# Kernel optimization log

Hardware: AMD Instinct MI355X
Metric: run time of the kernel (lower is better)

The kernel has to match this reference:

```python
import jax, jax.numpy as jnp
import numpy as np

B, N, DIM = 4, 4096, 1024
HEADS, DIM_HEAD, BSZ, EPS = 8, 64, 16, 1e-8
INNER = HEADS * DIM_HEAD


def setup_inputs() -> dict:
    key = jax.random.key(0)
    k1, k2, k3 = jax.random.split(key, 3)
    x = jax.random.normal(k1, (B, N, DIM), dtype=jnp.float32)
    # torch nn.Linear weights are [out, in]; scale ~ fan_in^-0.5 for stable exp()
    w_qkv = jax.random.normal(k2, (3 * INNER, DIM), dtype=jnp.float32) * (DIM ** -0.5)
    w_out = jax.random.normal(k3, (DIM, INNER), dtype=jnp.float32) * (INNER ** -0.5)
    b_out = jnp.zeros((DIM,), dtype=jnp.float32)
    return {"x": x, "w_qkv": w_qkv, "w_out": w_out, "b_out": b_out}


def _to_bh(t, b, n):
    # 'b n (h d) -> (b h) n d'
    return t.reshape(b, n, HEADS, DIM_HEAD).transpose(0, 2, 1, 3).reshape(b * HEADS, n, DIM_HEAD)


def _to_blocks(t):
    # 'b (n z) d -> b n z d'
    return t.reshape(t.shape[0], -1, BSZ, DIM_HEAD)


def _calc_Y_and_A(qb, kb, vb):
    S = jnp.einsum('bnid,bnjd->bnij', qb, kb)   # block-local scores
    A = jnp.exp(S)
    y = jnp.einsum('bnij,bnjd->bnid', A, vb)
    return y.reshape(y.shape[0], -1, DIM_HEAD), A.sum(-1).reshape(A.shape[0], -1)


def _hattention(x, w_qkv, w_out, b_out):
    b, n, _ = x.shape
    qkv = x @ w_qkv.T
    q, k, v = jnp.split(qkv, 3, axis=-1)
    q, k, v = (_to_bh(t, b, n) for t in (q, k, v))
    q = q * (DIM_HEAD ** -0.5)

    num_levels = int(np.log2(n // BSZ)) - 1
    qkvs = [(q, k, v)]
    for _ in range(num_levels):
        q = q.reshape(q.shape[0], -1, 2, DIM_HEAD).mean(axis=2)
        k = k.reshape(k.shape[0], -1, 2, DIM_HEAD).mean(axis=2)
        v = v.reshape(v.shape[0], -1, 2, DIM_HEAD).sum(axis=2)
        qkvs.append((q, k, v))
    top_level = qkvs[0]
    coarse_levels = qkvs[1:][::-1]  # coarsest first

    Ys = []
    for (ql, kl, vl) in coarse_levels:
        qb, kb, vb = map(_to_blocks, (ql, kl, vl))
        bh, nb = kb.shape[0], kb.shape[1]
        # flip sibling key blocks: 'b (n r) z d' with r=2 reversed
        kb = kb.reshape(bh, nb // 2, 2, BSZ, DIM_HEAD)[:, :, ::-1].reshape(bh, nb, BSZ, DIM_HEAD)
        Ys.append(_calc_Y_and_A(qb, kb, vb))
    Ys.append(_calc_Y_and_A(*map(_to_blocks, top_level)))

    Y, A = Ys[0]
    for y_l, a_l in Ys[1:]:
        Y = jnp.repeat(Y, 2, axis=1) + y_l
        A = jnp.repeat(A, 2, axis=1) + a_l

    out = Y / (A + EPS)[..., None]
    # '(b h) n d -> b n (h d)'
    out = out.reshape(b, HEADS, n, DIM_HEAD).transpose(0, 2, 1, 3).reshape(b, n, INNER)
    return out @ w_out.T + b_out


def reference(x, w_qkv, w_out, b_out):
    return _hattention(x, w_qkv, w_out, b_out)
```

## Files before the change

### kernel.cpp

```cpp
#include <hip/hip_runtime.h>
#include <hip/hip_bf16.h>


typedef __bf16 bf16x8 __attribute__((ext_vector_type(8)));
typedef float floatx4 __attribute__((ext_vector_type(4)));
typedef unsigned short ushortx8 __attribute__((ext_vector_type(8)));
typedef unsigned int uintx4 __attribute__((ext_vector_type(4)));

#define ROWS_PER_BH 8160

__device__ __forceinline__ void g2lds16(const void* g, void* l) {
  __builtin_amdgcn_global_load_lds(
      (const __attribute__((address_space(1))) void*)g,
      (__attribute__((address_space(3))) void*)l, 16, 0, 0);
}

__device__ __forceinline__ unsigned short f2bu(float x) {
  __hip_bfloat16 h = __float2bfloat16(x);
  return *(unsigned short*)&h;
}
__device__ __forceinline__ float bu2f(unsigned short u) {
  __hip_bfloat16 h = *(__hip_bfloat16*)&u;
  return __bfloat162float(h);
}

__global__ __launch_bounds__(256) void f2b3_kernel(const float* __restrict__ x,
                                                   const float* __restrict__ wq,
                                                   const float* __restrict__ wo,
                                                   __hip_bfloat16* __restrict__ xb,
                                                   __hip_bfloat16* __restrict__ wqb,
                                                   __hip_bfloat16* __restrict__ wob) {
  int i0 = (blockIdx.x * 256 + threadIdx.x) * 4;
  const float* s;
  __hip_bfloat16* d;
  if (i0 < 16777216) {
    s = x; d = xb;
  } else if (i0 < 16777216 + 1572864) {
    s = wq + (i0 - 16777216); d = wqb + (i0 - 16777216); i0 = 0;
    float4 v = *(const float4*)s;
    d[0] = __float2bfloat16(v.x); d[1] = __float2bfloat16(v.y);
    d[2] = __float2bfloat16(v.z); d[3] = __float2bfloat16(v.w);
    return;
  } else {
    s = wo + (i0 - 16777216 - 1572864); d = wob + (i0 - 16777216 - 1572864);
    float4 v = *(const float4*)s;
    d[0] = __float2bfloat16(v.x); d[1] = __float2bfloat16(v.y);
    d[2] = __float2bfloat16(v.z); d[3] = __float2bfloat16(v.w);
    return;
  }
  float4 v = *(const float4*)(s + i0);
  d[i0 + 0] = __float2bfloat16(v.x);
  d[i0 + 1] = __float2bfloat16(v.y);
  d[i0 + 2] = __float2bfloat16(v.z);
  d[i0 + 3] = __float2bfloat16(v.w);
}

template <int K>
__device__ __forceinline__ void gemm_core(const unsigned short* __restrict__ A,
                                          const unsigned short* __restrict__ B,
                                          unsigned short* ldsA, unsigned short* ldsB,
                                          int tM, int tN, floatx4 acc[4][4]) {
  const int tid = threadIdx.x;
  const int lane = tid & 63, w = tid >> 6;
  const int wm = w >> 1, wn = w & 1;
  const int lr = lane >> 3;
  const int gch = (lane & 7) ^ lr;
  const unsigned short* Ag = A + (size_t)(tM + w * 32 + lr) * K + gch * 8;
  const unsigned short* Bg = B + (size_t)(tN + w * 32 + lr) * K + gch * 8;
  unsigned short* lA = &ldsA[w * 2048 + lane * 8];
  unsigned short* lB = &ldsB[w * 2048 + lane * 8];

  const int rA = wm * 64 + (lane & 15);
  const int rB = wn * 64 + (lane & 15);
  const int quad = lane >> 4;
  const int sw = lane & 7;

  for (int kt = 0; kt < K; kt += 64) {
    __syncthreads();
#pragma unroll
    for (int c = 0; c < 4; c++) {
      g2lds16(Ag + (size_t)(c * 8) * K + kt, lA + c * 512);
      g2lds16(Bg + (size_t)(c * 8) * K + kt, lB + c * 512);
    }
    __syncthreads();
#pragma unroll
    for (int kk = 0; kk < 2; kk++) {
      bf16x8 af[4], bv[4];
#pragma unroll
      for (int i = 0; i < 4; i++)
        af[i] = *(const bf16x8*)&ldsA[(rA + i * 16) * 64 + (((kk * 4 + quad) ^ sw) * 8)];
#pragma unroll
      for (int j = 0; j < 4; j++)
        bv[j] = *(const bf16x8*)&ldsB[(rB + j * 16) * 64 + (((kk * 4 + quad) ^ sw) * 8)];
#pragma unroll
      for (int i = 0; i < 4; i++)
#pragma unroll
        for (int j = 0; j < 4; j++)
          acc[i][j] = __builtin_amdgcn_mfma_f32_16x16x32_bf16(af[i], bv[j], acc[i][j], 0, 0, 0);
    }
  }
}

__global__ __launch_bounds__(256) void gemm_qkv_kernel(
    const unsigned short* __restrict__ A,
    const unsigned short* __restrict__ B,
    __hip_bfloat16* __restrict__ qp, __hip_bfloat16* __restrict__ kp,
    __hip_bfloat16* __restrict__ vp) {
  __shared__ unsigned short ldsA[128 * 64];
  __shared__ unsigned short ldsB[128 * 64];
  const int lane = threadIdx.x & 63, w = threadIdx.x >> 6;
  const int wm = w >> 1, wn = w & 1;
  const int tM = blockIdx.x * 128, tN = blockIdx.y * 128;

  floatx4 acc[4][4];
#pragma unroll
  for (int i = 0; i < 4; i++)
#pragma unroll
    for (int j = 0; j < 4; j++) acc[i][j] = (floatx4){0.f, 0.f, 0.f, 0.f};

  gemm_core<1024>(A, B, ldsA, ldsB, tM, tN, acc);

  const int quad = lane >> 4;
#pragma unroll
  for (int i = 0; i < 4; i++) {
#pragma unroll
    for (int j = 0; j < 4; j++) {
      const int c = tN + wn * 64 + j * 16 + (lane & 15);
      const int tensor = c >> 9;
      const int rem = c & 511;
      const int h = rem >> 6, d = rem & 63;
      __hip_bfloat16* dstbuf = (tensor == 0) ? qp : ((tensor == 1) ? kp : vp);
      const float scale = (tensor == 0) ? 0.125f : 1.0f;
#pragma unroll
      for (int r = 0; r < 4; r++) {
        const int m = tM + wm * 64 + i * 16 + quad * 4 + r;
        const int b = m >> 12, n = m & 4095;
        size_t dst = ((size_t)(b * 8 + h) * ROWS_PER_BH + n) * 64 + d;
        dstbuf[dst] = __float2bfloat16(acc[i][j][r] * scale);
      }
    }
  }
}

__global__ __launch_bounds__(256) void gemm_out_kernel(
    const unsigned short* __restrict__ A,
    const unsigned short* __restrict__ B,
    const float* __restrict__ bias, float* __restrict__ out) {
  __shared__ unsigned short ldsA[128 * 64];
  __shared__ unsigned short ldsB[128 * 64];
  const int lane = threadIdx.x & 63, w = threadIdx.x >> 6;
  const int wm = w >> 1, wn = w & 1;
  const int tM = blockIdx.x * 128, tN = blockIdx.y * 128;

  floatx4 acc[4][4];
#pragma unroll
  for (int i = 0; i < 4; i++)
#pragma unroll
    for (int j = 0; j < 4; j++) acc[i][j] = (floatx4){0.f, 0.f, 0.f, 0.f};

  gemm_core<512>(A, B, ldsA, ldsB, tM, tN, acc);

  const int quad = lane >> 4;
#pragma unroll
  for (int i = 0; i < 4; i++) {
#pragma unroll
    for (int j = 0; j < 4; j++) {
      const int c = tN + wn * 64 + j * 16 + (lane & 15);
      const float bb = bias[c];
#pragma unroll
      for (int r = 0; r < 4; r++) {
        const int m = tM + wm * 64 + i * 16 + quad * 4 + r;
        out[(size_t)m * 1024 + c] = acc[i][j][r] + bb;
      }
    }
  }
}

__global__ __launch_bounds__(256) void pyramid_all_kernel(
    __hip_bfloat16* __restrict__ qp, __hip_bfloat16* __restrict__ kp,
    __hip_bfloat16* __restrict__ vp) {
  __shared__ unsigned short qs[128 * 64], ks[128 * 64], vs[128 * 64];
  const int bh = blockIdx.x >> 5;
  const int chunk = blockIdx.x & 31;
  const int tid = threadIdx.x;
  const size_t base = (size_t)bh * ROWS_PER_BH;
  const size_t g0 = (base + chunk * 128) * 64;
  const unsigned short* qg = (const unsigned short*)qp;
  const unsigned short* kg = (const unsigned short*)kp;
  const unsigned short* vg = (const unsigned short*)vp;
#pragma unroll
  for (int c = 0; c < 4; c++) {
    int off = c * 2048 + tid * 8;
    *(ushortx8*)&qs[off] = *(const ushortx8*)(qg + g0 + off);
    *(ushortx8*)&ks[off] = *(const ushortx8*)(kg + g0 + off);
    *(ushortx8*)&vs[off] = *(const ushortx8*)(vg + g0 + off);
  }
  const int offs[8] = {0, 4096, 6144, 7168, 7680, 7936, 8064, 8128};
#pragma unroll
  for (int l = 1; l <= 7; l++) {
    __syncthreads();
    const int nOut = 128 >> l;
    for (int e = tid; e < nOut * 32; e += 256) {
      const int i = e >> 5, dp = (e & 31) * 2;
      const int a = (i << l) * 64 + dp;
      const int b = a + (1 << (l - 1)) * 64;
      unsigned short q0 = f2bu(0.5f * (bu2f(qs[a]) + bu2f(qs[b])));
      unsigned short q1 = f2bu(0.5f * (bu2f(qs[a + 1]) + bu2f(qs[b + 1])));
      unsigned short k0 = f2bu(0.5f * (bu2f(ks[a]) + bu2f(ks[b])));
      unsigned short k1 = f2bu(0.5f * (bu2f(ks[a + 1]) + bu2f(ks[b + 1])));
      unsigned short v0 = f2bu(bu2f(vs[a]) + bu2f(vs[b]));
      unsigned short v1 = f2bu(bu2f(vs[a + 1]) + bu2f(vs[b + 1]));
      qs[a] = q0; qs[a + 1] = q1;
      ks[a] = k0; ks[a + 1] = k1;
      vs[a] = v0; vs[a + 1] = v1;
      const size_t grow = (base + offs[l] + (size_t)chunk * nOut + i) * 64 + dp;
      *(unsigned int*)((unsigned short*)qp + grow) = (unsigned int)q0 | ((unsigned int)q1 << 16);
      *(unsigned int*)((unsigned short*)kp + grow) = (unsigned int)k0 | ((unsigned int)k1 << 16);
      *(unsigned int*)((unsigned short*)vp + grow) = (unsigned int)v0 | ((unsigned int)v1 << 16);
    }
  }
}

__global__ __launch_bounds__(256) void attn_kernel(
    const unsigned short* __restrict__ qp, const unsigned short* __restrict__ kp,
    const unsigned short* __restrict__ vp, __hip_bfloat16* __restrict__ yall,
    float* __restrict__ aall) {
  __shared__ __align__(16) unsigned short vT[4][64 * 24];
  const int w = threadIdx.x >> 6, lane = threadIdx.x & 63;
  const int g = blockIdx.x * 4 + w;
  if (g >= 510) return;
  const int bh = blockIdx.y;
  int level, blk;
  if (g < 256)      { level = 0; blk = g; }
  else if (g < 384) { level = 1; blk = g - 256; }
  else if (g < 448) { level = 2; blk = g - 384; }
  else if (g < 480) { level = 3; blk = g - 448; }
  else if (g < 496) { level = 4; blk = g - 480; }
  else if (g < 504) { level = 5; blk = g - 496; }
  else if (g < 508) { level = 6; blk = g - 504; }
  else              { level = 7; blk = g - 508; }
  const int ro = 8192 - (8192 >> level);
  const int kblk = (level == 0) ? blk : (blk ^ 1);
  const int m = lane & 15, q = lane >> 4;
  const size_t qbase = ((size_t)bh * ROWS_PER_BH + ro + blk * 16) * 64;
  const size_t kbase = ((size_t)bh * ROWS_PER_BH + ro + kblk * 16) * 64;

  const bf16x8 ka0 = *(const bf16x8*)(kp + kbase + m * 64 + q * 8);
  const bf16x8 ka1 = *(const bf16x8*)(kp + kbase + m * 64 + 32 + q * 8);
  const bf16x8 qb0 = *(const bf16x8*)(qp + qbase + m * 64 + q * 8);
  const bf16x8 qb1 = *(const bf16x8*)(qp + qbase + m * 64 + 32 + q * 8);

  const ushortx8 v0 = *(const ushortx8*)(vp + qbase + m * 64 + q * 16);
  const ushortx8 v1 = *(const ushortx8*)(vp + qbase + m * 64 + q * 16 + 8);
  unsigned short* vtw = vT[w];
#pragma unroll
  for (int j = 0; j < 8; j++) vtw[(q * 16 + j) * 24 + m] = v0[j];
#pragma unroll
  for (int j = 0; j < 8; j++) vtw[(q * 16 + 8 + j) * 24 + m] = v1[j];

  floatx4 s = (floatx4){0.f, 0.f, 0.f, 0.f};
  s = __builtin_amdgcn_mfma_f32_16x16x32_bf16(ka0, qb0, s, 0, 0, 0);
  s = __builtin_amdgcn_mfma_f32_16x16x32_bf16(ka1, qb1, s, 0, 0, 0);

  unsigned short pb0 = f2bu(__expf(s[0])), pb1 = f2bu(__expf(s[1]));
  unsigned short pb2 = f2bu(__expf(s[2])), pb3 = f2bu(__expf(s[3]));
  float asum = bu2f(pb0) + bu2f(pb1) + bu2f(pb2) + bu2f(pb3);
  asum += __shfl_xor(asum, 16, 64);
  asum += __shfl_xor(asum, 32, 64);
  const size_t arow = (size_t)bh * ROWS_PER_BH + ro + blk * 16;
  if (q == 0) aall[arow + m] = asum;

  unsigned int d0 = (unsigned int)pb0 | ((unsigned int)pb1 << 16);
  unsigned int d1 = (unsigned int)pb2 | ((unsigned int)pb3 << 16);
  const int s0l = m + 32 * (q & 1);
  unsigned int u0 = __shfl(d0, s0l, 64);
  unsigned int u1 = __shfl(d1, s0l, 64);
  unsigned int u2 = __shfl(d0, s0l + 16, 64);
  unsigned int u3 = __shfl(d1, s0l + 16, 64);
  union { uintx4 i; bf16x8 b; } pau;
  pau.i = (q < 2) ? (uintx4){u0, u1, u2, u3} : (uintx4){0u, 0u, 0u, 0u};
  const bf16x8 pa = pau.b;

#pragma unroll
  for (int c = 0; c < 4; c++) {
    union { uintx4 i; bf16x8 b; } bvu;
    bvu.i = (uintx4){0u, 0u, 0u, 0u};
    if (q < 2) bvu.b = *(const bf16x8*)&vtw[(c * 16 + m) * 24 + q * 8];
    floatx4 y = (floatx4){0.f, 0.f, 0.f, 0.f};
    y = __builtin_amdgcn_mfma_f32_16x16x32_bf16(pa, bvu.b, y, 0, 0, 0);
#pragma unroll
    for (int r = 0; r < 4; r++)
      yall[(arow + q * 4 + r) * 64 + c * 16 + m] = __float2bfloat16(y[r]);
  }
}

__global__ __launch_bounds__(256) void combine_kernel(
    const unsigned short* __restrict__ yall, const float* __restrict__ aall,
    __hip_bfloat16* __restrict__ Ub) {
  int idx = blockIdx.x * 256 + threadIdx.x;
  int d4 = (idx & 15) * 4;
  int i = (idx >> 4) & 4095;
  int bh = idx >> 16;
  size_t base = (size_t)bh * ROWS_PER_BH;
  float Y0 = 0.f, Y1 = 0.f, Y2 = 0.f, Y3 = 0.f, Aa = 0.f;
#pragma unroll
  for (int l = 0; l < 8; l++) {
    int r = (8192 - (8192 >> l)) + (i >> l);
    uint2 yv = *(const uint2*)(yall + (base + r) * 64 + d4);
    Y0 += bu2f((unsigned short)(yv.x & 0xffff));
    Y1 += bu2f((unsigned short)(yv.x >> 16));
    Y2 += bu2f((unsigned short)(yv.y & 0xffff));
    Y3 += bu2f((unsigned short)(yv.y >> 16));
    Aa += aall[base + r];
  }
  float inv = 1.0f / (Aa + 1e-8f);
  unsigned int o0 = (unsigned int)f2bu(Y0 * inv) | ((unsigned int)f2bu(Y1 * inv) << 16);
  unsigned int o1 = (unsigned int)f2bu(Y2 * inv) | ((unsigned int)f2bu(Y3 * inv) << 16);
  int b = bh >> 3, h = bh & 7;
  size_t m = (size_t)b * 4096 + i;
  uint2 o = {o0, o1};
  *(uint2*)((unsigned short*)Ub + m * 512 + (size_t)h * 64 + d4) = o;
}

extern "C" void kernel_launch(void* const* d_in, const int* in_sizes, int n_in,
                              void* d_out, int out_size, void* d_ws, size_t ws_size,
                              hipStream_t stream) {
  const float* x     = (const float*)d_in[0];
  const float* w_qkv = (const float*)d_in[1];
  const float* w_out = (const float*)d_in[2];
  const float* b_out = (const float*)d_in[3];
  float* out = (float*)d_out;

  char* ws = (char*)d_ws;
  __hip_bfloat16* xb    = (__hip_bfloat16*)(ws + 0);
  __hip_bfloat16* wqkvb = (__hip_bfloat16*)(ws + 33554432);
  __hip_bfloat16* wob   = (__hip_bfloat16*)(ws + 36700160);
  __hip_bfloat16* qp    = (__hip_bfloat16*)(ws + 37748736);
  __hip_bfloat16* kp    = (__hip_bfloat16*)(ws + 71172096);
  __hip_bfloat16* vp    = (__hip_bfloat16*)(ws + 104595456);
  __hip_bfloat16* yall  = (__hip_bfloat16*)(ws + 138018816);
  float* aall           = (float*)(ws + 171442176);
  __hip_bfloat16* Ub    = (__hip_bfloat16*)(ws + 172486656);

  f2b3_kernel<<<18432, 256, 0, stream>>>(x, w_qkv, w_out, xb, wqkvb, wob);

  gemm_qkv_kernel<<<dim3(128, 12), 256, 0, stream>>>(
      (const unsigned short*)xb, (const unsigned short*)wqkvb, qp, kp, vp);

  pyramid_all_kernel<<<1024, 256, 0, stream>>>(qp, kp, vp);

  attn_kernel<<<dim3(128, 32), 256, 0, stream>>>(
      (const unsigned short*)qp, (const unsigned short*)kp,
      (const unsigned short*)vp, yall, aall);

  combine_kernel<<<8192, 256, 0, stream>>>((const unsigned short*)yall, aall, Ub);

  gemm_out_kernel<<<dim3(128, 8), 256, 0, stream>>>(
      (const unsigned short*)Ub, (const unsigned short*)wob, b_out, out);
}
```

Before: 264.7 us.

## Fuse fine pyramid levels, attention and combine into one LDS-resident kernel

The QKV GEMM epilogue now also writes level-4 (16-row mean/sum) pyramid rows directly using cross-lane shuffles. A small kernel builds levels 5-7 from those, a reduced attention kernel handles only coarse levels 4-7, and a new fused kernel loads a 256-row chunk per head into swizzled LDS, builds levels 1-3 in place, runs block attention for levels 0-3 and combines with the coarse results to write the normalized output. This removes the global round trips for fine pyramid levels and the per-level Y/A intermediates, at the cost of heavy LDS use (one block per CU) and low parallelism in the coarse-level kernels. Level-4 values now come from an fp32 sum over 16 rows rather than repeated bf16 pairwise averages, which shifts rounding.

```diff
diff --git a/kernel.cpp b/kernel.cpp
--- a/kernel.cpp
+++ b/kernel.cpp
@@ -36,7 +36,7 @@
   if (i0 < 16777216) {
     s = x; d = xb;
   } else if (i0 < 16777216 + 1572864) {
-    s = wq + (i0 - 16777216); d = wqb + (i0 - 16777216); i0 = 0;
+    s = wq + (i0 - 16777216); d = wqb + (i0 - 16777216);
     float4 v = *(const float4*)s;
     d[0] = __float2bfloat16(v.x); d[1] = __float2bfloat16(v.y);
     d[2] = __float2bfloat16(v.z); d[3] = __float2bfloat16(v.w);
@@ -120,12 +120,12 @@
 
   gemm_core<1024>(A, B, ldsA, ldsB, tM, tN, acc);
 
-  const int quad = lane >> 4;
+  const int quad = lane >> 4, m15 = lane & 15;
 #pragma unroll
   for (int i = 0; i < 4; i++) {
 #pragma unroll
     for (int j = 0; j < 4; j++) {
-      const int c = tN + wn * 64 + j * 16 + (lane & 15);
+      const int c = tN + wn * 64 + j * 16 + m15;
       const int tensor = c >> 9;
       const int rem = c & 511;
       const int h = rem >> 6, d = rem & 63;
@@ -137,6 +137,17 @@
         const int b = m >> 12, n = m & 4095;
         size_t dst = ((size_t)(b * 8 + h) * ROWS_PER_BH + n) * 64 + d;
         dstbuf[dst] = __float2bfloat16(acc[i][j][r] * scale);
+      }
+      float s4 = acc[i][j][0] + acc[i][j][1] + acc[i][j][2] + acc[i][j][3];
+      s4 += __shfl_xor(s4, 16, 64);
+      s4 += __shfl_xor(s4, 32, 64);
+      if (quad == 0) {
+        const int mrow = tM + wm * 64 + i * 16;
+        const int b = mrow >> 12, n4 = (mrow & 4095) >> 4;
+        const float val = (tensor == 0) ? s4 * (0.125f / 16.f)
+                         : ((tensor == 1) ? s4 * (1.f / 16.f) : s4);
+        dstbuf[((size_t)(b * 8 + h) * ROWS_PER_BH + 7680 + n4) * 64 + d] =
+            __float2bfloat16(val);
       }
     }
   }
@@ -176,30 +187,29 @@
   }
 }
 
-__global__ __launch_bounds__(256) void pyramid_all_kernel(
+__global__ __launch_bounds__(256) void pyramid47_kernel(
     __hip_bfloat16* __restrict__ qp, __hip_bfloat16* __restrict__ kp,
     __hip_bfloat16* __restrict__ vp) {
-  __shared__ unsigned short qs[128 * 64], ks[128 * 64], vs[128 * 64];
-  const int bh = blockIdx.x >> 5;
-  const int chunk = blockIdx.x & 31;
+  __shared__ unsigned short qs[256 * 64], ks[256 * 64], vs[256 * 64];
+  const int bh = blockIdx.x;
   const int tid = threadIdx.x;
   const size_t base = (size_t)bh * ROWS_PER_BH;
-  const size_t g0 = (base + chunk * 128) * 64;
+  const size_t g0 = (base + 7680) * 64;
   const unsigned short* qg = (const unsigned short*)qp;
   const unsigned short* kg = (const unsigned short*)kp;
   const unsigned short* vg = (const unsigned short*)vp;
 #pragma unroll
-  for (int c = 0; c < 4; c++) {
+  for (int c = 0; c < 8; c++) {
     int off = c * 2048 + tid * 8;
     *(ushortx8*)&qs[off] = *(const ushortx8*)(qg + g0 + off);
     *(ushortx8*)&ks[off] = *(const ushortx8*)(kg + g0 + off);
     *(ushortx8*)&vs[off] = *(const ushortx8*)(vg + g0 + off);
   }
-  const int offs[8] = {0, 4096, 6144, 7168, 7680, 7936, 8064, 8128};
-#pragma unroll
-  for (int l = 1; l <= 7; l++) {
+  const int offs[4] = {0, 7936, 8064, 8128};
+#pragma unroll
+  for (int l = 1; l <= 3; l++) {
     __syncthreads();
-    const int nOut = 128 >> l;
+    const int nOut = 256 >> l;
     for (int e = tid; e < nOut * 32; e += 256) {
       const int i = e >> 5, dp = (e & 31) * 2;
       const int a = (i << l) * 64 + dp;
@@ -213,7 +223,7 @@
       qs[a] = q0; qs[a + 1] = q1;
       ks[a] = k0; ks[a + 1] = k1;
       vs[a] = v0; vs[a + 1] = v1;
-      const size_t grow = (base + offs[l] + (size_t)chunk * nOut + i) * 64 + dp;
+      const size_t grow = (base + offs[l] + i) * 64 + dp;
       *(unsigned int*)((unsigned short*)qp + grow) = (unsigned int)q0 | ((unsigned int)q1 << 16);
       *(unsigned int*)((unsigned short*)kp + grow) = (unsigned int)k0 | ((unsigned int)k1 << 16);
       *(unsigned int*)((unsigned short*)vp + grow) = (unsigned int)v0 | ((unsigned int)v1 << 16);
@@ -221,26 +231,22 @@
   }
 }
 
-__global__ __launch_bounds__(256) void attn_kernel(
+__global__ __launch_bounds__(256) void attn47_kernel(
     const unsigned short* __restrict__ qp, const unsigned short* __restrict__ kp,
     const unsigned short* __restrict__ vp, __hip_bfloat16* __restrict__ yall,
     float* __restrict__ aall) {
   __shared__ __align__(16) unsigned short vT[4][64 * 24];
   const int w = threadIdx.x >> 6, lane = threadIdx.x & 63;
   const int g = blockIdx.x * 4 + w;
-  if (g >= 510) return;
+  if (g >= 30) return;
   const int bh = blockIdx.y;
   int level, blk;
-  if (g < 256)      { level = 0; blk = g; }
-  else if (g < 384) { level = 1; blk = g - 256; }
-  else if (g < 448) { level = 2; blk = g - 384; }
-  else if (g < 480) { level = 3; blk = g - 448; }
-  else if (g < 496) { level = 4; blk = g - 480; }
-  else if (g < 504) { level = 5; blk = g - 496; }
-  else if (g < 508) { level = 6; blk = g - 504; }
-  else              { level = 7; blk = g - 508; }
+  if (g < 16)      { level = 4; blk = g; }
+  else if (g < 24) { level = 5; blk = g - 16; }
+  else if (g < 28) { level = 6; blk = g - 24; }
+  else             { level = 7; blk = g - 28; }
   const int ro = 8192 - (8192 >> level);
-  const int kblk = (level == 0) ? blk : (blk ^ 1);
+  const int kblk = blk ^ 1;
   const int m = lane & 15, q = lane >> 4;
   const size_t qbase = ((size_t)bh * ROWS_PER_BH + ro + blk * 16) * 64;
   const size_t kbase = ((size_t)bh * ROWS_PER_BH + ro + kblk * 16) * 64;
@@ -294,32 +300,201 @@
   }
 }
 
-__global__ __launch_bounds__(256) void combine_kernel(
-    const unsigned short* __restrict__ yall, const float* __restrict__ aall,
-    __hip_bfloat16* __restrict__ Ub) {
-  int idx = blockIdx.x * 256 + threadIdx.x;
-  int d4 = (idx & 15) * 4;
-  int i = (idx >> 4) & 4095;
-  int bh = idx >> 16;
-  size_t base = (size_t)bh * ROWS_PER_BH;
-  float Y0 = 0.f, Y1 = 0.f, Y2 = 0.f, Y3 = 0.f, Aa = 0.f;
-#pragma unroll
-  for (int l = 0; l < 8; l++) {
-    int r = (8192 - (8192 >> l)) + (i >> l);
-    uint2 yv = *(const uint2*)(yall + (base + r) * 64 + d4);
-    Y0 += bu2f((unsigned short)(yv.x & 0xffff));
-    Y1 += bu2f((unsigned short)(yv.x >> 16));
-    Y2 += bu2f((unsigned short)(yv.y & 0xffff));
-    Y3 += bu2f((unsigned short)(yv.y >> 16));
-    Aa += aall[base + r];
-  }
-  float inv = 1.0f / (Aa + 1e-8f);
-  unsigned int o0 = (unsigned int)f2bu(Y0 * inv) | ((unsigned int)f2bu(Y1 * inv) << 16);
-  unsigned int o1 = (unsigned int)f2bu(Y2 * inv) | ((unsigned int)f2bu(Y3 * inv) << 16);
-  int b = bh >> 3, h = bh & 7;
-  size_t m = (size_t)b * 4096 + i;
-  uint2 o = {o0, o1};
-  *(uint2*)((unsigned short*)Ub + m * 512 + (size_t)h * 64 + d4) = o;
+__global__ __launch_bounds__(256, 1) void fused03_kernel(
+    const unsigned short* __restrict__ qp, const unsigned short* __restrict__ kp,
+    const unsigned short* __restrict__ vp, const unsigned short* __restrict__ yall,
+    const float* __restrict__ aall, __hip_bfloat16* __restrict__ Ub) {
+  __shared__ __align__(16) unsigned short qs[256 * 64];
+  __shared__ __align__(16) unsigned short ks[256 * 64];
+  __shared__ __align__(16) unsigned short vs[256 * 64];
+  __shared__ unsigned short ylds[224 * 72];
+  __shared__ float alds[480];
+  __shared__ __align__(16) unsigned short vT[4][64 * 24];
+
+  const int tid = threadIdx.x;
+  const int w = tid >> 6, lane = tid & 63;
+  const int m = lane & 15, q = lane >> 4;
+  const int c = blockIdx.x, bh = blockIdx.y;
+  const size_t base = (size_t)bh * ROWS_PER_BH;
+  const size_t g0 = (base + c * 256) * 64;
+
+  auto sidx = [](int r, int d) {
+    return r * 64 + (((d >> 3) ^ (r & 7)) << 3) + (d & 7);
+  };
+  unsigned short* vtw = vT[w];
+
+  {
+    const int srow = tid >> 3;
+    const int sch = (tid & 7) ^ (srow & 7);
+    const size_t gofs = (size_t)srow * 64 + sch * 8;
+#pragma unroll
+    for (int it = 0; it < 8; it++) {
+      const size_t gi = g0 + (size_t)it * 2048 + gofs;
+      g2lds16(qp + gi, &qs[it * 2048 + tid * 8]);
+      g2lds16(kp + gi, &ks[it * 2048 + tid * 8]);
+      g2lds16(vp + gi, &vs[it * 2048 + tid * 8]);
+    }
+  }
+  __syncthreads();
+
+  auto attn_block = [&](int level, int blk, bool flip, floatx4 yout[4]) -> float {
+    const int kb = flip ? (blk ^ 1) : blk;
+    const int Rq = (blk * 16 + m) << level;
+    const int Rk = (kb * 16 + m) << level;
+    const bf16x8 ka0 = *(const bf16x8*)&ks[sidx(Rk, q * 8)];
+    const bf16x8 ka1 = *(const bf16x8*)&ks[sidx(Rk, 32 + q * 8)];
+    const bf16x8 qb0 = *(const bf16x8*)&qs[sidx(Rq, q * 8)];
+    const bf16x8 qb1 = *(const bf16x8*)&qs[sidx(Rq, 32 + q * 8)];
+    const ushortx8 v0 = *(const ushortx8*)&vs[sidx(Rq, q * 16)];
+    const ushortx8 v1 = *(const ushortx8*)&vs[sidx(Rq, q * 16 + 8)];
+#pragma unroll
+    for (int j = 0; j < 8; j++) vtw[(q * 16 + j) * 24 + m] = v0[j];
+#pragma unroll
+    for (int j = 0; j < 8; j++) vtw[(q * 16 + 8 + j) * 24 + m] = v1[j];
+
+    floatx4 s = (floatx4){0.f, 0.f, 0.f, 0.f};
+    s = __builtin_amdgcn_mfma_f32_16x16x32_bf16(ka0, qb0, s, 0, 0, 0);
+    s = __builtin_amdgcn_mfma_f32_16x16x32_bf16(ka1, qb1, s, 0, 0, 0);
+
+    unsigned short pb0 = f2bu(__expf(s[0])), pb1 = f2bu(__expf(s[1]));
+    unsigned short pb2 = f2bu(__expf(s[2])), pb3 = f2bu(__expf(s[3]));
+    float asum = bu2f(pb0) + bu2f(pb1) + bu2f(pb2) + bu2f(pb3);
+    asum += __shfl_xor(asum, 16, 64);
+    asum += __shfl_xor(asum, 32, 64);
+
+    unsigned int d0 = (unsigned int)pb0 | ((unsigned int)pb1 << 16);
+    unsigned int d1 = (unsigned int)pb2 | ((unsigned int)pb3 << 16);
+    const int s0l = m + 32 * (q & 1);
+    unsigned int u0 = __shfl(d0, s0l, 64);
+    unsigned int u1 = __shfl(d1, s0l, 64);
+    unsigned int u2 = __shfl(d0, s0l + 16, 64);
+    unsigned int u3 = __shfl(d1, s0l + 16, 64);
+    union { uintx4 i; bf16x8 b; } pau;
+    pau.i = (q < 2) ? (uintx4){u0, u1, u2, u3} : (uintx4){0u, 0u, 0u, 0u};
+    const bf16x8 pa = pau.b;
+
+#pragma unroll
+    for (int cc = 0; cc < 4; cc++) {
+      union { uintx4 i; bf16x8 b; } bvu;
+      bvu.i = (uintx4){0u, 0u, 0u, 0u};
+      if (q < 2) bvu.b = *(const bf16x8*)&vtw[(cc * 16 + m) * 24 + q * 8];
+      floatx4 y = (floatx4){0.f, 0.f, 0.f, 0.f};
+      y = __builtin_amdgcn_mfma_f32_16x16x32_bf16(pa, bvu.b, y, 0, 0, 0);
+      yout[cc] = y;
+    }
+    return asum;
+  };
+
+  auto pyr = [&](int l) {
+    const int nOut = 256 >> l;
+    for (int e = tid; e < nOut * 32; e += 256) {
+      const int i = e >> 5, dp = (e & 31) * 2;
+      const int ra = i << l, rb = ra + (1 << (l - 1));
+      const int ia = sidx(ra, dp), ib = sidx(rb, dp);
+      unsigned short q0 = f2bu(0.5f * (bu2f(qs[ia]) + bu2f(qs[ib])));
+      unsigned short q1 = f2bu(0.5f * (bu2f(qs[ia + 1]) + bu2f(qs[ib + 1])));
+      unsigned short k0 = f2bu(0.5f * (bu2f(ks[ia]) + bu2f(ks[ib])));
+      unsigned short k1 = f2bu(0.5f * (bu2f(ks[ia + 1]) + bu2f(ks[ib + 1])));
+      unsigned short v0 = f2bu(bu2f(vs[ia]) + bu2f(vs[ib]));
+      unsigned short v1 = f2bu(bu2f(vs[ia + 1]) + bu2f(vs[ib + 1]));
+      qs[ia] = q0; qs[ia + 1] = q1;
+      ks[ia] = k0; ks[ia + 1] = k1;
+      vs[ia] = v0; vs[ia + 1] = v1;
+    }
+  };
+
+  floatx4 y0reg[4][4];
+#pragma unroll
+  for (int t = 0; t < 4; t++) {
+    const int blk = w + t * 4;
+    float a0 = attn_block(0, blk, false, y0reg[t]);
+    if (q == 0) alds[224 + blk * 16 + m] = a0;
+  }
+  __syncthreads();
+
+  pyr(1);
+  __syncthreads();
+  {
+    floatx4 yt[4];
+#pragma unroll
+    for (int t = 0; t < 2; t++) {
+      const int blk = w + t * 4;
+      float a = attn_block(1, blk, true, yt);
+      if (q == 0) alds[blk * 16 + m] = a;
+#pragma unroll
+      for (int cc = 0; cc < 4; cc++)
+#pragma unroll
+        for (int r = 0; r < 4; r++)
+          ylds[(blk * 16 + q * 4 + r) * 72 + cc * 16 + m] = f2bu(yt[cc][r]);
+    }
+  }
+  __syncthreads();
+  pyr(2);
+  __syncthreads();
+  {
+    floatx4 yt[4];
+    const int blk = w;
+    float a = attn_block(2, blk, true, yt);
+    if (q == 0) alds[128 + blk * 16 + m] = a;
+#pragma unroll
+    for (int cc = 0; cc < 4; cc++)
+#pragma unroll
+      for (int r = 0; r < 4; r++)
+        ylds[(128 + blk * 16 + q * 4 + r) * 72 + cc * 16 + m] = f2bu(yt[cc][r]);
+  }
+  __syncthreads();
+  pyr(3);
+  __syncthreads();
+  if (w < 2) {
+    floatx4 yt[4];
+    const int blk = w;
+    float a = attn_block(3, blk, true, yt);
+    if (q == 0) alds[192 + blk * 16 + m] = a;
+#pragma unroll
+    for (int cc = 0; cc < 4; cc++)
+#pragma unroll
+      for (int r = 0; r < 4; r++)
+        ylds[(192 + blk * 16 + q * 4 + r) * 72 + cc * 16 + m] = f2bu(yt[cc][r]);
+  }
+  __syncthreads();
+
+  const int bO = bh >> 3, hO = bh & 7;
+#pragma unroll
+  for (int t = 0; t < 4; t++) {
+    const int blk = w + t * 4;
+    const int i4 = c * 16 + blk;
+    const size_t r4 = base + 7680 + i4;
+    const size_t r5 = base + 7936 + (i4 >> 1);
+    const size_t r6 = base + 8064 + (i4 >> 2);
+    const size_t r7 = base + 8128 + (i4 >> 3);
+    const float acoarse = aall[r4] + aall[r5] + aall[r6] + aall[r7];
+
+    float inv[4];
+#pragma unroll
+    for (int r = 0; r < 4; r++) {
+      const int row = blk * 16 + q * 4 + r;
+      const float atot = alds[224 + row] + alds[row >> 1] +
+                         alds[128 + (row >> 2)] + alds[192 + (row >> 3)] +
+                         acoarse + 1e-8f;
+      inv[r] = 1.0f / atot;
+    }
+
+#pragma unroll
+    for (int cc = 0; cc < 4; cc++) {
+      const int col = cc * 16 + m;
+      const float yc = bu2f(yall[r4 * 64 + col]) + bu2f(yall[r5 * 64 + col]) +
+                       bu2f(yall[r6 * 64 + col]) + bu2f(yall[r7 * 64 + col]);
+#pragma unroll
+      for (int r = 0; r < 4; r++) {
+        const int row = blk * 16 + q * 4 + r;
+        const float num = y0reg[t][cc][r] + bu2f(ylds[(row >> 1) * 72 + col]) +
+                          bu2f(ylds[(128 + (row >> 2)) * 72 + col]) +
+                          bu2f(ylds[(192 + (row >> 3)) * 72 + col]) + yc;
+        Ub[((size_t)bO * 4096 + c * 256 + row) * 512 + hO * 64 + col] =
+            __float2bfloat16(num * inv[r]);
+      }
+    }
+  }
 }
 
 extern "C" void kernel_launch(void* const* d_in, const int* in_sizes, int n_in,
@@ -347,13 +522,15 @@
   gemm_qkv_kernel<<<dim3(128, 12), 256, 0, stream>>>(
       (const unsigned short*)xb, (const unsigned short*)wqkvb, qp, kp, vp);
 
-  pyramid_all_kernel<<<1024, 256, 0, stream>>>(qp, kp, vp);
-
-  attn_kernel<<<dim3(128, 32), 256, 0, stream>>>(
+  pyramid47_kernel<<<32, 256, 0, stream>>>(qp, kp, vp);
+
+  attn47_kernel<<<dim3(8, 32), 256, 0, stream>>>(
       (const unsigned short*)qp, (const unsigned short*)kp,
       (const unsigned short*)vp, yall, aall);
 
-  combine_kernel<<<8192, 256, 0, stream>>>((const unsigned short*)yall, aall, Ub);
+  fused03_kernel<<<dim3(16, 32), 256, 0, stream>>>(
+      (const unsigned short*)qp, (const unsigned short*)kp,
+      (const unsigned short*)vp, (const unsigned short*)yall, aall, Ub);
 
   gemm_out_kernel<<<dim3(128, 8), 256, 0, stream>>>(
       (const unsigned short*)Ub, (const unsigned short*)wob, b_out, out);
```

New measurement: 262.9 us. Within noise of the previous version (-0.7%).
